# Kernel tuning notes

Hardware: AMD Instinct MI355X
Metric: run time of the kernel (lower is better)

The kernel has to match this reference:

```python
import jax, jax.numpy as jnp
from jax import lax
import numpy as np

B, L, D_MODEL = 2, 2048, 1024
D_INNER, D_STATE, D_CONV, DT_RANK = 2048, 16, 4, 64


def setup_inputs() -> dict:
    key = jax.random.key(0)
    ks = jax.random.split(key, 10)
    s = 0.02  # weight scale to keep activations numerically sane
    return {
        "x": jax.random.normal(ks[0], (B, L, D_MODEL), jnp.float32),
        "W_in": jax.random.normal(ks[1], (D_MODEL, 2 * D_INNER), jnp.float32) * s,
        "conv_w": jax.random.normal(ks[2], (D_INNER, D_CONV), jnp.float32) * 0.2,
        "conv_b": jax.random.normal(ks[3], (D_INNER,), jnp.float32) * 0.1,
        "W_xproj": jax.random.normal(ks[4], (D_INNER, DT_RANK + 2 * D_STATE), jnp.float32) * s,
        "W_dt": jax.random.normal(ks[5], (DT_RANK, D_INNER), jnp.float32) * (DT_RANK ** -0.5),
        "b_dt": jax.random.normal(ks[6], (D_INNER,), jnp.float32) * 0.1,
        "A_log": jax.random.uniform(ks[7], (D_INNER, D_STATE), jnp.float32),
        "D_skip": jnp.ones((D_INNER,), jnp.float32),
        "W_out": jax.random.normal(ks[8], (D_INNER, D_MODEL), jnp.float32) * s,
    }


def _causal_depthwise_conv(xt, w, b):
    # xt: (B, L, d_inner), w: (d_inner, d_conv). Torch pads both sides by d_conv-1
    # then slices [:L] => causal left-pad of d_conv-1.
    xc = jnp.moveaxis(xt, 1, 2)  # (B, d_inner, L)
    out = lax.conv_general_dilated(
        xc, w[:, None, :], window_strides=(1,),
        padding=[(D_CONV - 1, 0)], feature_group_count=D_INNER)
    return jnp.moveaxis(out, 1, 2) + b  # (B, L, d_inner)


def _selective_scan(u, delta, A, Bm, Cm, D_skip):
    # u, delta: (B, L, d_inner); A: (d_inner, d_state); Bm, Cm: (B, L, d_state)
    deltaA = jnp.exp(delta[..., None] * A)                  # (B,L,di,ds)
    dBu = (delta * u)[..., None] * Bm[:, :, None, :]        # (B,L,di,ds)

    def step(h, inp):
        dA_t, dBu_t, C_t = inp                              # (B,di,ds),(B,di,ds),(B,ds)
        h = dA_t * h + dBu_t
        y = jnp.einsum('bds,bs->bd', h, C_t)
        return h, y

    h0 = jnp.zeros((u.shape[0], D_INNER, D_STATE), u.dtype)
    xs = (jnp.moveaxis(deltaA, 1, 0), jnp.moveaxis(dBu, 1, 0), jnp.moveaxis(Cm, 1, 0))
    _, ys = lax.scan(step, h0, xs)                          # ys: (L,B,di)
    return jnp.moveaxis(ys, 0, 1) + u * D_skip


def reference(x, W_in, conv_w, conv_b, W_xproj, W_dt, b_dt, A_log, D_skip, W_out):
    xz = x @ W_in                                           # (B,L,2*di)
    xin, z = jnp.split(xz, 2, axis=-1)
    xc = jax.nn.silu(_causal_depthwise_conv(xin, conv_w, conv_b))
    dbc = xc @ W_xproj                                      # (B,L,dt_rank+2*ds)
    dt_lo = dbc[..., :DT_RANK]
    Bm = dbc[..., DT_RANK:DT_RANK + D_STATE]
    Cm = dbc[..., DT_RANK + D_STATE:]
    delta = jax.nn.softplus(dt_lo @ W_dt + b_dt)            # (B,L,di)
    A = -jnp.exp(A_log)
    y = _selective_scan(xc, delta, A, Bm, Cm, D_skip)
    return (y * jax.nn.silu(z)) @ W_out                     # (B,L,d_model)
```

## Files before the change

### kernel.cpp

```cpp
#include <hip/hip_runtime.h>
#include <math.h>

#define B_SZ 2
#define L_SZ 2048
#define DMODEL 1024
#define DINNER 2048
#define DSTATE 16
#define DCONV 4
#define DTRANK 64

#define CS 32
#define NCH (L_SZ / CS)

typedef float f32x4 __attribute__((ext_vector_type(4)));
typedef float f32x2 __attribute__((ext_vector_type(2)));
typedef __bf16 bf16x8 __attribute__((ext_vector_type(8)));

__device__ __forceinline__ float silu_f(float x) {
    return x / (1.0f + __expf(-x));
}

__device__ __forceinline__ float softplus_f(float x) {
    return fmaxf(x, 0.0f) + __logf(1.0f + __expf(-fabsf(x)));
}

__device__ __forceinline__ float fexp2(float x) {
    float r;
    asm("v_exp_f32 %0, %1" : "=v"(r) : "v"(x));
    return r;
}

__device__ __forceinline__ unsigned short f2bf(float x) {
    unsigned int u = __float_as_uint(x);
    u = u + 0x7FFFu + ((u >> 16) & 1u);
    return (unsigned short)(u >> 16);
}

__device__ __forceinline__ float bf2f(unsigned short s) {
    return __uint_as_float(((unsigned int)s) << 16);
}

__device__ __forceinline__ void gload_lds16(const unsigned short* g, unsigned short* l) {
    __builtin_amdgcn_global_load_lds(
        (const __attribute__((address_space(1))) void*)g,
        (__attribute__((address_space(3))) void*)l, 16, 0, 0);
}

union Pack8 { unsigned short s[8]; uint4 v; };

__global__ __launch_bounds__(256) void transpose_cast(
    const float* __restrict__ W, unsigned short* __restrict__ WT, int R, int C)
{
    __shared__ float t[32][33];
    const int tx = threadIdx.x & 31;
    const int ty = threadIdx.x >> 5;
    const int r0 = blockIdx.y * 32;
    const int c0 = blockIdx.x * 32;
    #pragma unroll
    for (int i = 0; i < 4; i++)
        t[ty + i * 8][tx] = W[(r0 + ty + i * 8) * C + c0 + tx];
    __syncthreads();
    #pragma unroll
    for (int i = 0; i < 4; i++)
        WT[(c0 + ty + i * 8) * R + r0 + tx] = f2bf(t[tx][ty + i * 8]);
}

__global__ __launch_bounds__(256) void cast_bf16(
    const float* __restrict__ src, unsigned short* __restrict__ dst, int n8)
{
    int i = blockIdx.x * 256 + threadIdx.x;
    if (i >= n8) return;
    const float4 f0 = *(const float4*)(src + i * 8);
    const float4 f1 = *(const float4*)(src + i * 8 + 4);
    Pack8 p;
    p.s[0] = f2bf(f0.x); p.s[1] = f2bf(f0.y); p.s[2] = f2bf(f0.z); p.s[3] = f2bf(f0.w);
    p.s[4] = f2bf(f1.x); p.s[5] = f2bf(f1.y); p.s[6] = f2bf(f1.z); p.s[7] = f2bf(f1.w);
    *(uint4*)(dst + i * 8) = p.v;
}

template <int ACT, int OBF16>
__global__ __launch_bounds__(256) void gemm_bt_lds(
    const unsigned short* __restrict__ A, const unsigned short* __restrict__ BT,
    void* __restrict__ Cout, const float* __restrict__ bias,
    int M, int N, int K, int lda, int ldb, int ldc, int Kc)
{
    __shared__ unsigned short As[128 * 64];
    __shared__ unsigned short Bs[128 * 64];

    const int tid  = threadIdx.x;
    const int lane = tid & 63;
    const int wave = tid >> 6;
    const int wm   = wave >> 1;
    const int wn   = wave & 1;
    const int row0 = blockIdx.y * 128;
    const int col0 = blockIdx.x * 128;
    const int lq   = lane >> 4;
    const int lm   = lane & 15;
    const int kbeg = blockIdx.z * Kc;

    const int rloc = wave * 32 + (lane >> 3);
    const int sc   = (lane & 7) ^ ((lane >> 3) & 7);
    const unsigned short* gA = A + (size_t)(row0 + rloc) * lda + sc * 8;
    const unsigned short* gBp[4];
    #pragma unroll
    for (int is = 0; is < 4; is++) {
        int br = col0 + rloc + 8 * is;
        if (br > N - 1) br = N - 1;
        gBp[is] = BT + (size_t)br * ldb + sc * 8;
    }
    unsigned short* lA = As + wave * 2048;
    unsigned short* lB = Bs + wave * 2048;

    f32x4 acc[4][4];
    #pragma unroll
    for (int i = 0; i < 4; i++)
        #pragma unroll
        for (int j = 0; j < 4; j++)
            #pragma unroll
            for (int r = 0; r < 4; r++) acc[i][j][r] = 0.0f;

    for (int k0 = kbeg; k0 < kbeg + Kc; k0 += 64) {
        #pragma unroll
        for (int is = 0; is < 4; is++) {
            gload_lds16(gA + (size_t)(8 * is) * lda + k0, lA + is * 512);
            gload_lds16(gBp[is] + k0, lB + is * 512);
        }
        __syncthreads();

        #pragma unroll
        for (int ks = 0; ks < 2; ks++) {
            bf16x8 af[4], bfr[4];
            #pragma unroll
            for (int i = 0; i < 4; i++) {
                int row = wm * 64 + i * 16 + lm;
                af[i] = *(const bf16x8*)&As[row * 64 + (((ks * 4 + lq) ^ (row & 7)) * 8)];
            }
            #pragma unroll
            for (int j = 0; j < 4; j++) {
                int row = wn * 64 + j * 16 + lm;
                bfr[j] = *(const bf16x8*)&Bs[row * 64 + (((ks * 4 + lq) ^ (row & 7)) * 8)];
            }
            #pragma unroll
            for (int i = 0; i < 4; i++)
                #pragma unroll
                for (int j = 0; j < 4; j++)
                    acc[i][j] = __builtin_amdgcn_mfma_f32_16x16x32_bf16(
                        af[i], bfr[j], acc[i][j], 0, 0, 0);
        }
        __syncthreads();
    }

    #pragma unroll
    for (int i = 0; i < 4; i++) {
        #pragma unroll
        for (int r = 0; r < 4; r++) {
            int row = row0 + wm * 64 + i * 16 + lq * 4 + r;
            #pragma unroll
            for (int j = 0; j < 4; j++) {
                int col = col0 + wn * 64 + j * 16 + lm;
                if (col < N) {
                    float v = acc[i][j][r];
                    if (ACT == 1) v = softplus_f(v + bias[col]);
                    if (OBF16) {
                        unsigned short* Cz = (unsigned short*)Cout +
                            (size_t)blockIdx.z * (size_t)M * ldc;
                        Cz[(size_t)row * ldc + col] = f2bf(v);
                    } else {
                        float* Cz = (float*)Cout +
                            (size_t)blockIdx.z * (size_t)M * ldc;
                        Cz[(size_t)row * ldc + col] = v;
                    }
                }
            }
        }
    }
}

template <int OBF16>
__global__ __launch_bounds__(512, 2) void gemm_8ph(
    const unsigned short* __restrict__ A, const unsigned short* __restrict__ BT,
    void* __restrict__ Cout, int M, int N, int lda, int ldb, int ldc, int Kc)
{
    __shared__ unsigned short sm[2][2][4][64 * 64];

    const int tid  = threadIdx.x;
    const int lane = tid & 63;
    const int wave = tid >> 6;
    const int wm   = wave >> 2;
    const int wn   = wave & 3;
    const int lq   = lane >> 4;
    const int lm   = lane & 15;

    const int cpx = gridDim.x >> 3;
    const int ti  = (blockIdx.x & 7) * cpx + (blockIdx.x >> 3);
    const int nbx = N >> 8;
    const int row0 = (ti / nbx) * 256;
    const int col0 = (ti % nbx) * 256;
    const int kbeg = blockIdx.z * Kc;

    const int r  = tid >> 3;
    const int sc = (tid & 7) ^ (r & 7);
    const unsigned short* gA = A + (size_t)(row0 + r) * lda + sc * 8 + kbeg;
    const unsigned short* gB[4];
    #pragma unroll
    for (int u = 0; u < 4; u++) {
        int br = col0 + u * 64 + r;
        if (br > N - 1) br = N - 1;
        gB[u] = BT + (size_t)br * ldb + sc * 8 + kbeg;
    }

    #define STA(bsel, u, kk) gload_lds16(gA + (size_t)((u) * 64) * lda + (kk), \
                                         &sm[bsel][0][u][wave * 512])
    #define STB(bsel, u, kk) gload_lds16(gB[u] + (kk), &sm[bsel][1][u][wave * 512])

    f32x4 acc[8][4];
    #pragma unroll
    for (int i = 0; i < 8; i++)
        #pragma unroll
        for (int j = 0; j < 4; j++)
            #pragma unroll
            for (int rr = 0; rr < 4; rr++) acc[i][j][rr] = 0.0f;

    const int NT = Kc >> 6;
    STB(0, 0, 0); STB(0, 1, 0); STA(0, 0, 0); STA(0, 2, 0);
    STA(0, 1, 0); STA(0, 3, 0); STB(0, 2, 0); STB(0, 3, 0);
    if (NT > 1) { STB(1, 0, 64); STB(1, 1, 64); STA(1, 0, 64); STA(1, 2, 64); }

    bf16x8 bq[4][2];

    for (int t = 0; t < NT; ++t) {
        const int b   = t & 1;
        const int kk1 = (t + 1) * 64;
        const int kk2 = (t + 2) * 64;

        if (t == NT - 1) asm volatile("s_waitcnt vmcnt(0)" ::: "memory");
        else             asm volatile("s_waitcnt vmcnt(4)" ::: "memory");
        __builtin_amdgcn_s_barrier();
        __builtin_amdgcn_sched_barrier(0);

        #pragma unroll
        for (int q = 0; q < 4; ++q) {
            bf16x8 af2[2][2];
            #pragma unroll
            for (int ii = 0; ii < 2; ii++) {
                int br = wm * 128 + (2 * q + ii) * 16 + lm;
                #pragma unroll
                for (int ks = 0; ks < 2; ks++)
                    af2[ii][ks] = *(const bf16x8*)&sm[b][0][br >> 6]
                        [(br & 63) * 64 + (((ks * 4 + lq) ^ (br & 7)) * 8)];
            }
            if (q == 0) {
                #pragma unroll
                for (int j = 0; j < 4; j++) {
                    int br = wn * 64 + j * 16 + lm;
                    #pragma unroll
                    for (int ks = 0; ks < 2; ks++)
                        bq[j][ks] = *(const bf16x8*)&sm[b][1][br >> 6]
                            [(br & 63) * 64 + (((ks * 4 + lq) ^ (br & 7)) * 8)];
                }
            }
            if (q == 0 && t + 1 < NT) { STA(b ^ 1, 1, kk1); STA(b ^ 1, 3, kk1); }
            if (q == 1 && t + 1 < NT) { STB(b ^ 1, 2, kk1); STB(b ^ 1, 3, kk1); }
            if (q == 2 && t + 2 < NT) { STB(b, 0, kk2); STB(b, 1, kk2); }
            if (q == 3 && t + 2 < NT) { STA(b, 0, kk2); STA(b, 2, kk2); }

            asm volatile("s_waitcnt lgkmcnt(0)" ::: "memory");
            __builtin_amdgcn_sched_barrier(0);
            __builtin_amdgcn_s_setprio(1);
            #pragma unroll
            for (int ii = 0; ii < 2; ii++)
                #pragma unroll
                for (int j = 0; j < 4; j++) {
                    acc[2 * q + ii][j] = __builtin_amdgcn_mfma_f32_16x16x32_bf16(
                        af2[ii][0], bq[j][0], acc[2 * q + ii][j], 0, 0, 0);
                    acc[2 * q + ii][j] = __builtin_amdgcn_mfma_f32_16x16x32_bf16(
                        af2[ii][1], bq[j][1], acc[2 * q + ii][j], 0, 0, 0);
                }
            __builtin_amdgcn_s_setprio(0);
            __builtin_amdgcn_sched_barrier(0);
            if (q < 3) {
                __builtin_amdgcn_s_barrier();
                __builtin_amdgcn_sched_barrier(0);
            }
        }
    }
    #undef STA
    #undef STB

    const size_t zoff = (size_t)blockIdx.z * (size_t)M * ldc;
    #pragma unroll
    for (int i = 0; i < 8; i++) {
        #pragma unroll
        for (int rr = 0; rr < 4; rr++) {
            int row = row0 + wm * 128 + i * 16 + lq * 4 + rr;
            #pragma unroll
            for (int j = 0; j < 4; j++) {
                int col = col0 + wn * 64 + j * 16 + lm;
                if (col < N) {
                    float v = acc[i][j][rr];
                    if (OBF16)
                        ((unsigned short*)Cout)[(size_t)row * ldc + col] = f2bf(v);
                    else
                        ((float*)Cout)[zoff + (size_t)row * ldc + col] = v;
                }
            }
        }
    }
}

__global__ __launch_bounds__(256) void reduce_splitk(
    const float* __restrict__ part, float* __restrict__ C,
    unsigned short* __restrict__ dtlo16, int n, int nsplit)
{
    int i = blockIdx.x * 256 + threadIdx.x;
    if (i >= n) return;
    float s = 0.0f;
    for (int z = 0; z < nsplit; z++) s += part[(size_t)z * n + i];
    C[i] = s;
    int row = i / 96;
    int col = i - row * 96;
    if (col < DTRANK) dtlo16[row * DTRANK + col] = f2bf(s);
}

__global__ __launch_bounds__(256) void reduce4(
    const float* __restrict__ part, float* __restrict__ out, int n4)
{
    int i = blockIdx.x * 256 + threadIdx.x;
    if (i >= n4) return;
    const f32x4* p = (const f32x4*)part;
    f32x4 s = p[i];
    s += p[i + n4];
    s += p[i + 2 * n4];
    s += p[i + 3 * n4];
    ((f32x4*)out)[i] = s;
}

__global__ __launch_bounds__(256) void conv_silu_v2(
    const unsigned short* __restrict__ xz16, const float* __restrict__ conv_w,
    const float* __restrict__ conv_b, unsigned short* __restrict__ xc16)
{
    const int tid = threadIdx.x;
    const int d   = blockIdx.x * 256 + tid;
    const int l0  = blockIdx.y * 32;
    const int b   = blockIdx.z;
    const float4 w  = *(const float4*)(conv_w + d * 4);
    const float bias = conv_b[d];
    const int t0 = b * L_SZ + l0;
    const unsigned short* src = xz16 + (size_t)t0 * 4096 + d;

    float r0, r1, r2;
    if (l0 == 0) {
        r0 = r1 = r2 = 0.0f;
    } else {
        r0 = bf2f(src[-3 * 4096]);
        r1 = bf2f(src[-2 * 4096]);
        r2 = bf2f(src[-1 * 4096]);
    }
    #pragma unroll 4
    for (int l = 0; l < 32; l++) {
        float r3 = bf2f(src[(size_t)l * 4096]);
        float acc = bias + r0 * w.x + r1 * w.y + r2 * w.z + r3 * w.w;
        xc16[(size_t)(t0 + l) * DINNER + d] = f2bf(silu_f(acc));
        r0 = r1; r1 = r2; r2 = r3;
    }
}

__global__ __launch_bounds__(256) void scan_pass1(
    const unsigned short* __restrict__ xc16, const float* __restrict__ delta,
    const float* __restrict__ dbc, const float* __restrict__ A_log,
    float* __restrict__ P, float* __restrict__ E)
{
    __shared__ float Bs[CS * DSTATE];
    const int tid = threadIdx.x;
    const int db  = blockIdx.x & 7;
    const int c   = (blockIdx.x >> 3) & (NCH - 1);
    const int b   = blockIdx.x >> 9;
    const int d   = db * 256 + tid;
    const int t0  = b * L_SZ + c * CS;

    for (int idx = tid; idx < CS * DSTATE; idx += 256) {
        int step = idx >> 4, i = idx & 15;
        Bs[idx] = dbc[(t0 + step) * 96 + DTRANK + i];
    }

    f32x2 A2v[8], Er2[8];
    const float* Ap = A_log + d * DSTATE;
    #pragma unroll
    for (int p = 0; p < 8; p++) {
        A2v[p].x = -1.44269504f * __expf(Ap[2 * p]);
        A2v[p].y = -1.44269504f * __expf(Ap[2 * p + 1]);
        Er2[p].x = 0.0f; Er2[p].y = 0.0f;
    }
    float sd = 0.0f;

    const float* dp = delta + (size_t)t0 * DINNER + d;
    const unsigned short* up = xc16 + (size_t)t0 * DINNER + d;

    float dv[4], uv[4];
    #pragma unroll
    for (int q = 0; q < 4; q++) {
        dv[q] = dp[(size_t)q * DINNER];
        uv[q] = bf2f(up[(size_t)q * DINNER]);
    }
    __syncthreads();

    for (int lo = 0; lo < CS; lo += 4) {
        float nd[4], nu[4];
        if (lo + 4 < CS) {
            #pragma unroll
            for (int q = 0; q < 4; q++) {
                nd[q] = dp[(size_t)(lo + 4 + q) * DINNER];
                nu[q] = bf2f(up[(size_t)(lo + 4 + q) * DINNER]);
            }
        }
        #pragma unroll
        for (int q = 0; q < 4; q++) {
            const float dvq = dv[q];
            const float du  = dvq * uv[q];
            sd += dvq;
            const f32x4* Bv = (const f32x4*)&Bs[(lo + q) * DSTATE];
            f32x4 b0 = Bv[0], b1 = Bv[1], b2 = Bv[2], b3 = Bv[3];
            #define P1PAIR(p, bb) { \
                f32x2 m = dvq * A2v[p]; \
                f32x2 e; e.x = fexp2(m.x); e.y = fexp2(m.y); \
                Er2[p] = e * Er2[p] + du * (bb); }
            P1PAIR(0, b0.xy) P1PAIR(1, b0.zw)
            P1PAIR(2, b1.xy) P1PAIR(3, b1.zw)
            P1PAIR(4, b2.xy) P1PAIR(5, b2.zw)
            P1PAIR(6, b3.xy) P1PAIR(7, b3.zw)
            #undef P1PAIR
        }
        #pragma unroll
        for (int q = 0; q < 4; q++) { dv[q] = nd[q]; uv[q] = nu[q]; }
    }

    const long long o = ((long long)((b * NCH + c) * DINNER) + d) * DSTATE;
    #pragma unroll
    for (int w = 0; w < 4; w++) {
        f32x4 pv, ev;
        #pragma unroll
        for (int k = 0; k < 2; k++) {
            int p = w * 2 + k;
            pv[2 * k]     = fexp2(A2v[p].x * sd);
            pv[2 * k + 1] = fexp2(A2v[p].y * sd);
            ev[2 * k]     = Er2[p].x;
            ev[2 * k + 1] = Er2[p].y;
        }
        *(f32x4*)(P + o + w * 4) = pv;
        *(f32x4*)(E + o + w * 4) = ev;
    }
}

__global__ __launch_bounds__(256) void scan_pass2(
    const float* __restrict__ P, float* __restrict__ E)
{
    const int gid  = blockIdx.x * 256 + threadIdx.x;
    const int b    = gid >> 15;
    const int rest = gid & 32767;
    float h = 0.0f;
    for (int c = 0; c < NCH; c++) {
        const long long idx = (long long)(b * NCH + c) * (DINNER * DSTATE) + rest;
        float p = P[idx];
        float e = E[idx];
        E[idx] = h;
        h = p * h + e;
    }
}

__global__ __launch_bounds__(256) void scan_pass3(
    const unsigned short* __restrict__ xc16, const float* __restrict__ delta,
    const float* __restrict__ dbc, const float* __restrict__ A_log,
    const float* __restrict__ D_skip, const float* __restrict__ Hin,
    const unsigned short* __restrict__ xz16, unsigned short* __restrict__ y16)
{
    __shared__ float BCs[CS * 2 * DSTATE];
    const int tid = threadIdx.x;
    const int db  = blockIdx.x & 7;
    const int c   = (blockIdx.x >> 3) & (NCH - 1);
    const int b   = blockIdx.x >> 9;
    const int d   = db * 256 + tid;
    const int t0  = b * L_SZ + c * CS;

    for (int idx = tid; idx < CS * 2 * DSTATE; idx += 256) {
        int step = idx >> 5, i = idx & 31;
        BCs[idx] = dbc[(t0 + step) * 96 + DTRANK + i];
    }

    f32x2 A2v[8], h2[8];
    const float* Ap = A_log + d * DSTATE;
    const long long o = ((long long)((b * NCH + c) * DINNER) + d) * DSTATE;
    #pragma unroll
    for (int p = 0; p < 8; p++) {
        A2v[p].x = -1.44269504f * __expf(Ap[2 * p]);
        A2v[p].y = -1.44269504f * __expf(Ap[2 * p + 1]);
        h2[p].x = Hin[o + 2 * p];
        h2[p].y = Hin[o + 2 * p + 1];
    }
    const float Dv = D_skip[d];

    const float* dp = delta + (size_t)t0 * DINNER + d;
    const unsigned short* up = xc16 + (size_t)t0 * DINNER + d;
    const unsigned short* zp = xz16 + (size_t)t0 * 4096 + DINNER + d;
    unsigned short* yp = y16 + (size_t)t0 * DINNER + d;

    float dv[4], uv[4], zv[4];
    #pragma unroll
    for (int q = 0; q < 4; q++) {
        dv[q] = dp[(size_t)q * DINNER];
        uv[q] = bf2f(up[(size_t)q * DINNER]);
        zv[q] = bf2f(zp[(size_t)q * 4096]);
    }
    __syncthreads();

    for (int lo = 0; lo < CS; lo += 4) {
        float nd[4], nu[4], nz[4];
        if (lo + 4 < CS) {
            #pragma unroll
            for (int q = 0; q < 4; q++) {
                nd[q] = dp[(size_t)(lo + 4 + q) * DINNER];
                nu[q] = bf2f(up[(size_t)(lo + 4 + q) * DINNER]);
                nz[q] = bf2f(zp[(size_t)(lo + 4 + q) * 4096]);
            }
        }
        #pragma unroll
        for (int q = 0; q < 4; q++) {
            const float dvq = dv[q];
            const float uvq = uv[q];
            const float du  = dvq * uvq;
            const f32x4* Bv = (const f32x4*)&BCs[(lo + q) * 32];
            f32x4 b0 = Bv[0], b1 = Bv[1], b2 = Bv[2], b3 = Bv[3];
            f32x4 c0 = Bv[4], c1 = Bv[5], c2 = Bv[6], c3 = Bv[7];
            f32x2 y0; y0.x = 0.0f; y0.y = 0.0f;
            f32x2 y1; y1.x = 0.0f; y1.y = 0.0f;
            #define P3PAIR(p, bb, cc, ya) { \
                f32x2 m = dvq * A2v[p]; \
                f32x2 e; e.x = fexp2(m.x); e.y = fexp2(m.y); \
                h2[p] = e * h2[p] + du * (bb); \
                ya = ya + h2[p] * (cc); }
            P3PAIR(0, b0.xy, c0.xy, y0) P3PAIR(1, b0.zw, c0.zw, y1)
            P3PAIR(2, b1.xy, c1.xy, y0) P3PAIR(3, b1.zw, c1.zw, y1)
            P3PAIR(4, b2.xy, c2.xy, y0) P3PAIR(5, b2.zw, c2.zw, y1)
            P3PAIR(6, b3.xy, c3.xy, y0) P3PAIR(7, b3.zw, c3.zw, y1)
            #undef P3PAIR
            f32x2 ys = y0 + y1;
            float yv = ys.x + ys.y;
            yp[(size_t)(lo + q) * DINNER] = f2bf((uvq * Dv + yv) * silu_f(zv[q]));
        }
        #pragma unroll
        for (int q = 0; q < 4; q++) { dv[q] = nd[q]; uv[q] = nu[q]; zv[q] = nz[q]; }
    }
}

extern "C" void kernel_launch(void* const* d_in, const int* in_sizes, int n_in,
                              void* d_out, int out_size, void* d_ws, size_t ws_size,
                              hipStream_t stream) {
    const float* x       = (const float*)d_in[0];
    const float* W_in    = (const float*)d_in[1];
    const float* conv_w  = (const float*)d_in[2];
    const float* conv_b  = (const float*)d_in[3];
    const float* W_xproj = (const float*)d_in[4];
    const float* W_dt    = (const float*)d_in[5];
    const float* b_dt    = (const float*)d_in[6];
    const float* A_log   = (const float*)d_in[7];
    const float* D_skip  = (const float*)d_in[8];
    const float* W_out   = (const float*)d_in[9];
    float* out = (float*)d_out;

    float* ws = (float*)d_ws;
    unsigned short* xz16   = (unsigned short*)ws;
    unsigned short* xc16   = (unsigned short*)(ws +  8388608);
    float* dbc             = ws + 12582912;
    unsigned short* dtlo16 = (unsigned short*)(ws + 12976128);
    float* delta           = ws + 13107200;
    float* Ebuf            = ws + 21495808;
    float* Pbuf            = ws + 25690112;
    float* parts           = Pbuf;
    float* parts6          = delta;
    unsigned short* yb16   = (unsigned short*)(ws + 29884416);
    unsigned short* x16    = yb16;
    unsigned short* W_inT    = (unsigned short*)(ws + 31981568);
    unsigned short* W_xprojT = (unsigned short*)(ws + 34078720);
    unsigned short* W_dtT    = (unsigned short*)(ws + 34177024);
    unsigned short* W_outT   = (unsigned short*)(ws + 34242560);

    const int MT = 4096;

    transpose_cast<<<dim3(128, 32), 256, 0, stream>>>(W_in,    W_inT,    1024, 4096);
    transpose_cast<<<dim3(  3, 64), 256, 0, stream>>>(W_xproj, W_xprojT, 2048,   96);
    transpose_cast<<<dim3( 64,  2), 256, 0, stream>>>(W_dt,    W_dtT,      64, 2048);
    transpose_cast<<<dim3( 32, 64), 256, 0, stream>>>(W_out,   W_outT,   2048, 1024);
    cast_bf16<<<dim3(2048), 256, 0, stream>>>(x, x16, 524288);

    gemm_8ph<1><<<dim3(256), 512, 0, stream>>>(
        x16, W_inT, xz16, MT, 4096, 1024, 1024, 4096, 1024);

    conv_silu_v2<<<dim3(8, 64, 2), 256, 0, stream>>>(xz16, conv_w, conv_b, xc16);

    gemm_bt_lds<0, 0><<<dim3(1, 32, 8), 256, 0, stream>>>(
        xc16, W_xprojT, parts, nullptr, MT, 96, 2048, 2048, 2048, 96, 256);
    reduce_splitk<<<dim3(1536), 256, 0, stream>>>(parts, dbc, dtlo16, MT * 96, 8);

    gemm_bt_lds<1, 0><<<dim3(16, 32), 256, 0, stream>>>(
        dtlo16, W_dtT, delta, b_dt, MT, 2048, 64, 64, 64, 2048, 64);

    scan_pass1<<<dim3(1024), 256, 0, stream>>>(xc16, delta, dbc, A_log, Pbuf, Ebuf);
    scan_pass2<<<dim3(256), 256, 0, stream>>>(Pbuf, Ebuf);
    scan_pass3<<<dim3(1024), 256, 0, stream>>>(xc16, delta, dbc, A_log, D_skip,
                                               Ebuf, xz16, yb16);

    gemm_8ph<0><<<dim3(64, 1, 4), 512, 0, stream>>>(
        yb16, W_outT, parts6, MT, 1024, 2048, 2048, 1024, 512);
    reduce4<<<dim3(4096), 256, 0, stream>>>(parts6, out, MT * 1024 / 4);
}
```

Before: 307.5 us.

## Double-buffer A fragments in registers to overlap LDS reads with MFMA

Restructures the GEMM inner loop so that A-fragment LDS reads for the next quarter are issued before the current quarter's MFMAs run, using two register fragment sets (afA/afB) in ping-pong. The explicit lgkmcnt(0) waits before each MFMA group are removed and the reads are placed around the barriers, so that LDS latency is meant to hide behind matrix work. This adds register pressure from the extra fragments. It also relies on the compiler inserting the right waitcnts, and on the ordering between the LDS reads and the async global-to-LDS stores into the buffer that is being reused.

```diff
diff --git a/kernel.cpp b/kernel.cpp
--- a/kernel.cpp
+++ b/kernel.cpp
@@ -213,6 +213,37 @@
                                          &sm[bsel][0][u][wave * 512])
     #define STB(bsel, u, kk) gload_lds16(gB[u] + (kk), &sm[bsel][1][u][wave * 512])
 
+    #define RDA(dst, bsel, pr) { \
+        _Pragma("unroll") \
+        for (int ii = 0; ii < 2; ii++) { \
+            int br = wm * 128 + ((pr) * 2 + ii) * 16 + lm; \
+            _Pragma("unroll") \
+            for (int ks = 0; ks < 2; ks++) \
+                dst[ii][ks] = *(const bf16x8*)&sm[bsel][0][br >> 6] \
+                    [(br & 63) * 64 + (((ks * 4 + lq) ^ (br & 7)) * 8)]; \
+        } }
+    #define RDB(bsel) { \
+        _Pragma("unroll") \
+        for (int j = 0; j < 4; j++) { \
+            int br = wn * 64 + j * 16 + lm; \
+            _Pragma("unroll") \
+            for (int ks = 0; ks < 2; ks++) \
+                bq[j][ks] = *(const bf16x8*)&sm[bsel][1][br >> 6] \
+                    [(br & 63) * 64 + (((ks * 4 + lq) ^ (br & 7)) * 8)]; \
+        } }
+    #define MMPH(af, p) { \
+        __builtin_amdgcn_s_setprio(1); \
+        _Pragma("unroll") \
+        for (int ii = 0; ii < 2; ii++) \
+            _Pragma("unroll") \
+            for (int j = 0; j < 4; j++) { \
+                acc[2 * (p) + ii][j] = __builtin_amdgcn_mfma_f32_16x16x32_bf16( \
+                    af[ii][0], bq[j][0], acc[2 * (p) + ii][j], 0, 0, 0); \
+                acc[2 * (p) + ii][j] = __builtin_amdgcn_mfma_f32_16x16x32_bf16( \
+                    af[ii][1], bq[j][1], acc[2 * (p) + ii][j], 0, 0, 0); \
+            } \
+        __builtin_amdgcn_s_setprio(0); }
+
     f32x4 acc[8][4];
     #pragma unroll
     for (int i = 0; i < 8; i++)
@@ -226,7 +257,7 @@
     STA(0, 1, 0); STA(0, 3, 0); STB(0, 2, 0); STB(0, 3, 0);
     if (NT > 1) { STB(1, 0, 64); STB(1, 1, 64); STA(1, 0, 64); STA(1, 2, 64); }
 
-    bf16x8 bq[4][2];
+    bf16x8 bq[4][2], afA[2][2], afB[2][2];
 
     for (int t = 0; t < NT; ++t) {
         const int b   = t & 1;
@@ -238,54 +269,38 @@
         __builtin_amdgcn_s_barrier();
         __builtin_amdgcn_sched_barrier(0);
 
-        #pragma unroll
-        for (int q = 0; q < 4; ++q) {
-            bf16x8 af2[2][2];
-            #pragma unroll
-            for (int ii = 0; ii < 2; ii++) {
-                int br = wm * 128 + (2 * q + ii) * 16 + lm;
-                #pragma unroll
-                for (int ks = 0; ks < 2; ks++)
-                    af2[ii][ks] = *(const bf16x8*)&sm[b][0][br >> 6]
-                        [(br & 63) * 64 + (((ks * 4 + lq) ^ (br & 7)) * 8)];
-            }
-            if (q == 0) {
-                #pragma unroll
-                for (int j = 0; j < 4; j++) {
-                    int br = wn * 64 + j * 16 + lm;
-                    #pragma unroll
-                    for (int ks = 0; ks < 2; ks++)
-                        bq[j][ks] = *(const bf16x8*)&sm[b][1][br >> 6]
-                            [(br & 63) * 64 + (((ks * 4 + lq) ^ (br & 7)) * 8)];
-                }
-            }
-            if (q == 0 && t + 1 < NT) { STA(b ^ 1, 1, kk1); STA(b ^ 1, 3, kk1); }
-            if (q == 1 && t + 1 < NT) { STB(b ^ 1, 2, kk1); STB(b ^ 1, 3, kk1); }
-            if (q == 2 && t + 2 < NT) { STB(b, 0, kk2); STB(b, 1, kk2); }
-            if (q == 3 && t + 2 < NT) { STA(b, 0, kk2); STA(b, 2, kk2); }
-
-            asm volatile("s_waitcnt lgkmcnt(0)" ::: "memory");
-            __builtin_amdgcn_sched_barrier(0);
-            __builtin_amdgcn_s_setprio(1);
-            #pragma unroll
-            for (int ii = 0; ii < 2; ii++)
-                #pragma unroll
-                for (int j = 0; j < 4; j++) {
-                    acc[2 * q + ii][j] = __builtin_amdgcn_mfma_f32_16x16x32_bf16(
-                        af2[ii][0], bq[j][0], acc[2 * q + ii][j], 0, 0, 0);
-                    acc[2 * q + ii][j] = __builtin_amdgcn_mfma_f32_16x16x32_bf16(
-                        af2[ii][1], bq[j][1], acc[2 * q + ii][j], 0, 0, 0);
-                }
-            __builtin_amdgcn_s_setprio(0);
-            __builtin_amdgcn_sched_barrier(0);
-            if (q < 3) {
-                __builtin_amdgcn_s_barrier();
-                __builtin_amdgcn_sched_barrier(0);
-            }
-        }
+        RDB(b);
+        RDA(afA, b, 0);
+        RDA(afB, b, 1);
+        if (t + 1 < NT) { STA(b ^ 1, 1, kk1); STA(b ^ 1, 3, kk1); }
+        MMPH(afA, 0);
+        RDA(afA, b, 2);
+        __builtin_amdgcn_sched_barrier(0);
+        __builtin_amdgcn_s_barrier();
+        __builtin_amdgcn_sched_barrier(0);
+
+        if (t + 1 < NT) { STB(b ^ 1, 2, kk1); STB(b ^ 1, 3, kk1); }
+        MMPH(afB, 1);
+        RDA(afB, b, 3);
+        __builtin_amdgcn_sched_barrier(0);
+        __builtin_amdgcn_s_barrier();
+        __builtin_amdgcn_sched_barrier(0);
+
+        if (t + 2 < NT) { STB(b, 0, kk2); STB(b, 1, kk2); }
+        MMPH(afA, 2);
+        __builtin_amdgcn_sched_barrier(0);
+        __builtin_amdgcn_s_barrier();
+        __builtin_amdgcn_sched_barrier(0);
+
+        if (t + 2 < NT) { STA(b, 0, kk2); STA(b, 2, kk2); }
+        MMPH(afB, 3);
+        __builtin_amdgcn_sched_barrier(0);
     }
     #undef STA
     #undef STB
+    #undef RDA
+    #undef RDB
+    #undef MMPH
 
     const size_t zoff = (size_t)blockIdx.z * (size_t)M * ldc;
     #pragma unroll
```

Result: no change. 302.4 us (-1.7%).
